# Kernel tuning notes

Hardware: AMD Instinct MI355X
Metric: run time of the kernel (lower is better)

The kernel has to match this reference:

```python
import jax, jax.numpy as jnp
import numpy as np

EPS = 1e-6  # flax LayerNorm default

def _layernorm(x, scale, bias):
    mu = jnp.mean(x, axis=-1, keepdims=True)
    var = jnp.mean(jnp.square(x - mu), axis=-1, keepdims=True)
    return (x - mu) * jax.lax.rsqrt(var + EPS) * scale + bias

def _rel_pos_index(ws):
    coords = np.stack(np.meshgrid(np.arange(ws), np.arange(ws), indexing='ij'))  # [2,ws,ws]
    cf = coords.reshape(2, -1)
    rel = (cf[:, :, None] - cf[:, None, :]).transpose(1, 2, 0)  # [N,N,2]
    rel[..., 0] += ws - 1
    rel[..., 1] += ws - 1
    rel[..., 0] *= 2 * ws - 1
    return rel.sum(-1)  # [N,N] in [0,(2ws-1)^2)

def setup_inputs() -> dict:
    key = jax.random.key(0)
    ks = jax.random.split(key, 8)
    B, H, W, C = 16, 56, 56, 384
    L, heads, ws = 2, 12, 7
    s = 0.02
    return {
        'x': jax.random.normal(ks[0], (B, H, W, C), jnp.float32),
        'ln1_s': jnp.ones((L, C), jnp.float32),
        'ln1_b': jnp.zeros((L, C), jnp.float32),
        'qkv_w': jax.random.normal(ks[1], (L, C, 3 * C), jnp.float32) * s,
        'rpb': jax.random.normal(ks[2], (L, (2 * ws - 1) ** 2, heads), jnp.float32) * s,
        'proj_w': jax.random.normal(ks[3], (L, C, C), jnp.float32) * s,
        'ln2_s': jnp.ones((L, C), jnp.float32),
        'ln2_b': jnp.zeros((L, C), jnp.float32),
        'mlp_w1': jax.random.normal(ks[4], (L, C, 4 * C), jnp.float32) * s,
        'mlp_b1': jnp.zeros((L, 4 * C), jnp.float32),
        'mlp_w2': jax.random.normal(ks[5], (L, 4 * C, C), jnp.float32) * s,
        'mlp_b2': jnp.zeros((L, C), jnp.float32),
        'window_size': 7,
    }

def reference(x, ln1_s, ln1_b, qkv_w, rpb, proj_w, ln2_s, ln2_b, mlp_w1, mlp_b1, mlp_w2, mlp_b2, window_size):
    B, H, W, C = x.shape
    ws = int(window_size)
    L = qkv_w.shape[0]
    heads = rpb.shape[-1]
    hd = C // heads
    N = ws * ws
    idx = jnp.asarray(_rel_pos_index(ws))  # [N,N] static

    # --- split to windows: [B,H,W,C] -> [B*nWh*nWw, N, C]
    xw = x.reshape(B, H // ws, ws, W // ws, ws, C)
    xw = xw.transpose(0, 1, 3, 2, 4, 5).reshape(-1, N, C)

    for l in range(L):
        # --- windowed MHSA with relative position bias
        h = _layernorm(xw, ln1_s[l], ln1_b[l])
        qkv = (h @ qkv_w[l]).reshape(-1, N, 3, heads, hd)
        q, k, v = qkv[:, :, 0], qkv[:, :, 1], qkv[:, :, 2]  # [nW,N,heads,hd]
        attn = jnp.einsum('wqhd,wkhd->whqk', q, k) * (hd ** -0.5)
        bias = rpb[l][idx].transpose(2, 0, 1)  # [heads,N,N]
        attn = jax.nn.softmax(attn + bias[None], axis=-1)
        o = jnp.einsum('whqk,wkhd->wqhd', attn, v).reshape(-1, N, C)
        xw = xw + o @ proj_w[l]
        # --- MLP block
        h = _layernorm(xw, ln2_s[l], ln2_b[l])
        h = jax.nn.gelu(h @ mlp_w1[l] + mlp_b1[l])
        xw = xw + (h @ mlp_w2[l] + mlp_b2[l])

    # --- merge windows back to [B,H,W,C]
    out = xw.reshape(B, H // ws, W // ws, ws, ws, C)
    out = out.transpose(0, 1, 3, 2, 4, 5).reshape(B, H, W, C)
    return out
```

## Files before the change

### kernel.cpp

```cpp
#include <hip/hip_runtime.h>
#include <hip/hip_bf16.h>

typedef __bf16 bf16;
typedef __attribute__((ext_vector_type(4))) __bf16 bf16x4;
typedef __attribute__((ext_vector_type(8))) __bf16 bf16x8;
typedef __attribute__((ext_vector_type(4))) float f32x4;

__device__ __forceinline__ void async_ld16(const void* g, void* l) {
    __builtin_amdgcn_global_load_lds(
        (const __attribute__((address_space(1))) unsigned int*)g,
        (__attribute__((address_space(3))) unsigned int*)l, 16, 0, 0);
}

__global__ __launch_bounds__(256) void k_f2bt(const float* __restrict__ in,
                                              bf16* __restrict__ out, int Kd, int Nd) {
    int id = blockIdx.x * 256 + threadIdx.x;
    if (id >= Kd * Nd) return;
    int k = id / Nd, n = id - k * Nd;
    out[(size_t)n * Kd + k] = (bf16)in[id];
}

__global__ __launch_bounds__(256) void k_reorder_in(const float4* __restrict__ x,
                                                    float4* __restrict__ xres) {
    int id = blockIdx.x * 256 + threadIdx.x;
    int c4 = id % 96;
    int t = id / 96;
    int b = t / 3136;
    int rem = t - b * 3136;
    int y = rem / 56;
    int xc = rem - y * 56;
    int w = b * 64 + (y / 7) * 8 + (xc / 7);
    int n = (y % 7) * 7 + (xc % 7);
    xres[(size_t)(w * 49 + n) * 96 + c4] = x[id];
}

__global__ __launch_bounds__(256) void k_reorder_out(const float4* __restrict__ xres,
                                                     float4* __restrict__ out) {
    int id = blockIdx.x * 256 + threadIdx.x;
    int c4 = id % 96;
    int t = id / 96;
    int b = t / 3136;
    int rem = t - b * 3136;
    int y = rem / 56;
    int xc = rem - y * 56;
    int w = b * 64 + (y / 7) * 8 + (xc / 7);
    int n = (y % 7) * 7 + (xc % 7);
    out[id] = xres[(size_t)(w * 49 + n) * 96 + c4];
}

__global__ __launch_bounds__(256) void k_ln(const float* __restrict__ xres,
                                            const float* __restrict__ s,
                                            const float* __restrict__ b,
                                            bf16* __restrict__ h) {
    int t = blockIdx.x * 4 + (threadIdx.x >> 6);
    int lane = threadIdx.x & 63;
    const float4* row = (const float4*)(xres + (size_t)t * 384);
    float4 v0 = row[lane];
    float4 v1 = make_float4(0.f, 0.f, 0.f, 0.f);
    if (lane < 32) v1 = row[64 + lane];
    float sum = v0.x + v0.y + v0.z + v0.w + v1.x + v1.y + v1.z + v1.w;
#pragma unroll
    for (int m = 1; m < 64; m <<= 1) sum += __shfl_xor(sum, m);
    float mu = sum * (1.f / 384.f);
    float sq = (v0.x - mu) * (v0.x - mu) + (v0.y - mu) * (v0.y - mu) +
               (v0.z - mu) * (v0.z - mu) + (v0.w - mu) * (v0.w - mu);
    if (lane < 32)
        sq += (v1.x - mu) * (v1.x - mu) + (v1.y - mu) * (v1.y - mu) +
              (v1.z - mu) * (v1.z - mu) + (v1.w - mu) * (v1.w - mu);
#pragma unroll
    for (int m = 1; m < 64; m <<= 1) sq += __shfl_xor(sq, m);
    float r = rsqrtf(sq * (1.f / 384.f) + 1e-6f);
    const float4* s4 = (const float4*)s;
    const float4* b4 = (const float4*)b;
    bf16* ho = h + (size_t)t * 384;
    {
        float4 sv = s4[lane], bv = b4[lane];
        bf16x4 ov;
        ov[0] = (bf16)((v0.x - mu) * r * sv.x + bv.x);
        ov[1] = (bf16)((v0.y - mu) * r * sv.y + bv.y);
        ov[2] = (bf16)((v0.z - mu) * r * sv.z + bv.z);
        ov[3] = (bf16)((v0.w - mu) * r * sv.w + bv.w);
        *(bf16x4*)&ho[lane * 4] = ov;
    }
    if (lane < 32) {
        float4 sv = s4[64 + lane], bv = b4[64 + lane];
        bf16x4 ov;
        ov[0] = (bf16)((v1.x - mu) * r * sv.x + bv.x);
        ov[1] = (bf16)((v1.y - mu) * r * sv.y + bv.y);
        ov[2] = (bf16)((v1.z - mu) * r * sv.z + bv.z);
        ov[3] = (bf16)((v1.w - mu) * r * sv.w + bv.w);
        *(bf16x4*)&ho[256 + lane * 4] = ov;
    }
}

__device__ inline float gelu_f(float x) {
    float u = 0.7978845608028654f * (x + 0.044715f * x * x * x);
    float t = 1.f - 2.f / (__expf(2.f * u) + 1.f);
    return 0.5f * x * (1.f + t);
}

template <int EPI>
__global__ __launch_bounds__(256) void k_gemm(const bf16* __restrict__ A,
                                              const bf16* __restrict__ Bt,
                                              const float* __restrict__ bias,
                                              float* __restrict__ resid,
                                              bf16* __restrict__ Cout,
                                              int N, int K) {
    __shared__ __align__(16) char lds[17408];
    bf16* As = (bf16*)lds;
    bf16* Bs = (bf16*)(lds + 8192);
    int tid = threadIdx.x;
    int n0 = blockIdx.x * 128;
    int m0 = blockIdx.y * 128;
    int wave = tid >> 6, lane = tid & 63;
    int wm = (wave >> 1) * 64, wn = (wave & 1) * 64;
    int col = lane & 15, quad = lane >> 4;

    f32x4 acc[4][4] = {};

    int r0 = 2 * wave * 16 + (lane >> 2);
    int ksl = (lane & 3) ^ ((r0 >> 1) & 3);
    const bf16* ga0 = A + (size_t)(m0 + r0) * K + ksl * 8;
    const bf16* gb0 = Bt + (size_t)(n0 + r0) * K + ksl * 8;
    size_t rowK16 = (size_t)16 * K;
    bf16* la0 = &As[2 * wave * 512];
    bf16* la1 = &As[(2 * wave + 1) * 512];
    bf16* lb0 = &Bs[2 * wave * 512];
    bf16* lb1 = &Bs[(2 * wave + 1) * 512];

    for (int kb = 0; kb < K; kb += 32) {
        __syncthreads();
        async_ld16(ga0 + kb, la0);
        async_ld16(ga0 + rowK16 + kb, la1);
        async_ld16(gb0 + kb, lb0);
        async_ld16(gb0 + rowK16 + kb, lb1);
        __syncthreads();

        bf16x8 af[4], bfv[4];
#pragma unroll
        for (int i = 0; i < 4; i++) {
            int ra = wm + i * 16 + col;
            af[i] = *(const bf16x8*)&As[ra * 32 + ((quad ^ ((ra >> 1) & 3)) << 3)];
            int rb = wn + i * 16 + col;
            bfv[i] = *(const bf16x8*)&Bs[rb * 32 + ((quad ^ ((rb >> 1) & 3)) << 3)];
        }
#pragma unroll
        for (int mi = 0; mi < 4; mi++)
#pragma unroll
            for (int ni = 0; ni < 4; ni++)
                acc[mi][ni] = __builtin_amdgcn_mfma_f32_16x16x32_bf16(
                    af[mi], bfv[ni], acc[mi][ni], 0, 0, 0);
    }

    __syncthreads();
    float* scrw = (float*)lds + wave * (16 * 68);

    int prow = lane >> 3;
    int pc0 = (lane & 7) * 8;
#pragma unroll
    for (int mi = 0; mi < 4; mi++) {
#pragma unroll
        for (int ni = 0; ni < 4; ni++)
#pragma unroll
            for (int r = 0; r < 4; r++)
                scrw[(quad * 4 + r) * 68 + ni * 16 + col] = acc[mi][ni][r];
#pragma unroll
        for (int h = 0; h < 2; h++) {
            int lr = h * 8 + prow;
            const float* sp = scrw + lr * 68 + pc0;
            float4 u0 = *(const float4*)sp;
            float4 u1 = *(const float4*)(sp + 4);
            int gm = m0 + wm + mi * 16 + lr;
            int gn = n0 + wn + pc0;
            size_t off = (size_t)gm * N + gn;
            if (EPI == 0) {
                bf16x8 ov;
                ov[0] = (bf16)u0.x; ov[1] = (bf16)u0.y; ov[2] = (bf16)u0.z; ov[3] = (bf16)u0.w;
                ov[4] = (bf16)u1.x; ov[5] = (bf16)u1.y; ov[6] = (bf16)u1.z; ov[7] = (bf16)u1.w;
                *(bf16x8*)&Cout[off] = ov;
            } else if (EPI == 1) {
                float4 b0 = *(const float4*)&bias[gn];
                float4 b1 = *(const float4*)&bias[gn + 4];
                bf16x8 ov;
                ov[0] = (bf16)gelu_f(u0.x + b0.x); ov[1] = (bf16)gelu_f(u0.y + b0.y);
                ov[2] = (bf16)gelu_f(u0.z + b0.z); ov[3] = (bf16)gelu_f(u0.w + b0.w);
                ov[4] = (bf16)gelu_f(u1.x + b1.x); ov[5] = (bf16)gelu_f(u1.y + b1.y);
                ov[6] = (bf16)gelu_f(u1.z + b1.z); ov[7] = (bf16)gelu_f(u1.w + b1.w);
                *(bf16x8*)&Cout[off] = ov;
            } else if (EPI == 2) {
                float4 r0v = *(const float4*)&resid[off];
                float4 r1v = *(const float4*)&resid[off + 4];
                r0v.x += u0.x; r0v.y += u0.y; r0v.z += u0.z; r0v.w += u0.w;
                r1v.x += u1.x; r1v.y += u1.y; r1v.z += u1.z; r1v.w += u1.w;
                *(float4*)&resid[off] = r0v;
                *(float4*)&resid[off + 4] = r1v;
            } else {
                float4 b0 = *(const float4*)&bias[gn];
                float4 b1 = *(const float4*)&bias[gn + 4];
                float4 r0v = *(const float4*)&resid[off];
                float4 r1v = *(const float4*)&resid[off + 4];
                r0v.x += u0.x + b0.x; r0v.y += u0.y + b0.y;
                r0v.z += u0.z + b0.z; r0v.w += u0.w + b0.w;
                r1v.x += u1.x + b1.x; r1v.y += u1.y + b1.y;
                r1v.z += u1.z + b1.z; r1v.w += u1.w + b1.w;
                *(float4*)&resid[off] = r0v;
                *(float4*)&resid[off + 4] = r1v;
            }
        }
    }
}

__global__ __launch_bounds__(256) void k_attn(const bf16* __restrict__ qkv,
                                              const float* __restrict__ rpb,
                                              bf16* __restrict__ o) {
    __shared__ unsigned short relIdx[2401];
    __shared__ float rpbs[4][169];
    __shared__ __align__(16) bf16 Vs[4][32 * 72];
    __shared__ __align__(16) bf16 Ps[4][64 * 72];

    int tid = threadIdx.x;
    int wave = tid >> 6, lane = tid & 63;
    int col = lane & 15, quad = lane >> 4;
    int w = blockIdx.x;
    int head = blockIdx.y * 4 + wave;
    const float scale = 0.17677669529663687f;

    for (int e = tid; e < 2401; e += 256) {
        int i = e / 49, j = e - i * 49;
        int yi = i / 7, xi = i - yi * 7, yj = j / 7, xj = j - yj * 7;
        relIdx[e] = (unsigned short)((yi - yj + 6) * 13 + (xi - xj + 6));
    }
    for (int e = lane; e < 169; e += 64) rpbs[wave][e] = rpb[e * 12 + head];

    const bf16* base = qkv + (size_t)w * 49 * 1152 + head * 32;
    bf16* vsw = Vs[wave];
    bf16* psw = Ps[wave];

    bf16x4 z4 = {(bf16)0.f, (bf16)0.f, (bf16)0.f, (bf16)0.f};
    for (int e = lane; e < 576; e += 64) *(bf16x4*)&vsw[e * 4] = z4;
    for (int e = lane; e < 392; e += 64) {
        int j = e >> 3, d4 = (e & 7) * 4;
        bf16x4 vv = *(const bf16x4*)&base[768 + (size_t)j * 1152 + d4];
        vsw[(d4 + 0) * 72 + j] = vv[0];
        vsw[(d4 + 1) * 72 + j] = vv[1];
        vsw[(d4 + 2) * 72 + j] = vv[2];
        vsw[(d4 + 3) * 72 + j] = vv[3];
    }

    __syncthreads();

    bf16x8 qf[4], kf[4];
#pragma unroll
    for (int mi = 0; mi < 4; mi++) {
        size_t row = (size_t)(mi * 16 + col) * 1152 + quad * 8;
        qf[mi] = *(const bf16x8*)&base[row];
        kf[mi] = *(const bf16x8*)&base[384 + row];
    }

    f32x4 S[4][4] = {};
#pragma unroll
    for (int mi = 0; mi < 4; mi++)
#pragma unroll
        for (int nj = 0; nj < 4; nj++)
            S[mi][nj] = __builtin_amdgcn_mfma_f32_16x16x32_bf16(qf[mi], kf[nj], S[mi][nj], 0, 0, 0);

    float* rp = rpbs[wave];
#pragma unroll
    for (int mi = 0; mi < 4; mi++) {
#pragma unroll
        for (int r = 0; r < 4; r++) {
            int ii = mi * 16 + quad * 4 + r;
            int ir = (ii < 49 ? ii : 0) * 49;
            float sv[4];
            float mx = -1e30f;
#pragma unroll
            for (int nj = 0; nj < 4; nj++) {
                int j = nj * 16 + col;
                float v;
                if (j < 49) v = S[mi][nj][r] * scale + rp[relIdx[ir + j]];
                else v = -1e30f;
                sv[nj] = v;
                mx = fmaxf(mx, v);
            }
#pragma unroll
            for (int m = 1; m < 16; m <<= 1) mx = fmaxf(mx, __shfl_xor(mx, m));
            float sum = 0.f;
#pragma unroll
            for (int nj = 0; nj < 4; nj++) {
                float p = __expf(sv[nj] - mx);
                sv[nj] = p;
                sum += p;
            }
#pragma unroll
            for (int m = 1; m < 16; m <<= 1) sum += __shfl_xor(sum, m);
            float is = 1.f / sum;
#pragma unroll
            for (int nj = 0; nj < 4; nj++)
                psw[ii * 72 + nj * 16 + col] = (bf16)(sv[nj] * is);
        }
    }

    __syncthreads();

    f32x4 O[4][2] = {};
#pragma unroll
    for (int kt = 0; kt < 2; kt++) {
        bf16x8 vb[2];
#pragma unroll
        for (int nt = 0; nt < 2; nt++)
            vb[nt] = *(const bf16x8*)&vsw[(nt * 16 + col) * 72 + kt * 32 + quad * 8];
#pragma unroll
        for (int mi = 0; mi < 4; mi++) {
            bf16x8 pa = *(const bf16x8*)&psw[(mi * 16 + col) * 72 + kt * 32 + quad * 8];
#pragma unroll
            for (int nt = 0; nt < 2; nt++)
                O[mi][nt] = __builtin_amdgcn_mfma_f32_16x16x32_bf16(pa, vb[nt], O[mi][nt], 0, 0, 0);
        }
    }

    bf16* ob = o + (size_t)w * 49 * 384 + head * 32;
#pragma unroll
    for (int mi = 0; mi < 4; mi++) {
#pragma unroll
        for (int r = 0; r < 4; r++) {
            int i = mi * 16 + quad * 4 + r;
            if (i < 49) {
#pragma unroll
                for (int nt = 0; nt < 2; nt++)
                    ob[(size_t)i * 384 + nt * 16 + col] = (bf16)O[mi][nt][r];
            }
        }
    }
}

extern "C" void kernel_launch(void* const* d_in, const int* in_sizes, int n_in,
                              void* d_out, int out_size, void* d_ws, size_t ws_size,
                              hipStream_t stream) {
    const float* x      = (const float*)d_in[0];
    const float* ln1_s  = (const float*)d_in[1];
    const float* ln1_b  = (const float*)d_in[2];
    const float* qkv_w  = (const float*)d_in[3];
    const float* rpb    = (const float*)d_in[4];
    const float* proj_w = (const float*)d_in[5];
    const float* ln2_s  = (const float*)d_in[6];
    const float* ln2_b  = (const float*)d_in[7];
    const float* mlp_w1 = (const float*)d_in[8];
    const float* mlp_b1 = (const float*)d_in[9];
    const float* mlp_w2 = (const float*)d_in[10];
    const float* mlp_b2 = (const float*)d_in[11];
    float* out = (float*)d_out;

    char* ws = (char*)d_ws;
    float* xres  = (float*)ws;
    bf16* qkvbuf = (bf16*)(ws + 77070336);
    bf16* obuf   = (bf16*)(ws + 192675840);
    bf16* wbuf   = (bf16*)(ws + 231211008);
    bf16* hidden = qkvbuf;
    bf16* hbuf   = (bf16*)d_out;

    bf16* qkvw_b  = wbuf;
    bf16* projw_b = wbuf + 884736;
    bf16* mlp1_b  = wbuf + 1179648;
    bf16* mlp2_b  = wbuf + 2359296;

    for (int l = 0; l < 2; l++) {
        k_f2bt<<<1728, 256, 0, stream>>>(qkv_w + (size_t)l * 442368,
                                         qkvw_b + (size_t)l * 442368, 384, 1152);
        k_f2bt<<<576, 256, 0, stream>>>(proj_w + (size_t)l * 147456,
                                        projw_b + (size_t)l * 147456, 384, 384);
        k_f2bt<<<2304, 256, 0, stream>>>(mlp_w1 + (size_t)l * 589824,
                                         mlp1_b + (size_t)l * 589824, 384, 1536);
        k_f2bt<<<2304, 256, 0, stream>>>(mlp_w2 + (size_t)l * 589824,
                                         mlp2_b + (size_t)l * 589824, 1536, 384);
    }

    k_reorder_in<<<18816, 256, 0, stream>>>((const float4*)x, (float4*)xres);

    for (int l = 0; l < 2; l++) {
        k_ln<<<12544, 256, 0, stream>>>(xres, ln1_s + l * 384, ln1_b + l * 384, hbuf);
        k_gemm<0><<<dim3(9, 392), 256, 0, stream>>>(
            hbuf, qkvw_b + (size_t)l * 442368, nullptr, nullptr, qkvbuf, 1152, 384);
        k_attn<<<dim3(1024, 3), 256, 0, stream>>>(qkvbuf, rpb + l * 169 * 12, obuf);
        k_gemm<2><<<dim3(3, 392), 256, 0, stream>>>(
            obuf, projw_b + (size_t)l * 147456, nullptr, xres, nullptr, 384, 384);
        k_ln<<<12544, 256, 0, stream>>>(xres, ln2_s + l * 384, ln2_b + l * 384, hbuf);
        k_gemm<1><<<dim3(12, 392), 256, 0, stream>>>(
            hbuf, mlp1_b + (size_t)l * 589824, mlp_b1 + l * 1536, nullptr, hidden, 1536, 384);
        k_gemm<3><<<dim3(3, 392), 256, 0, stream>>>(
            hidden, mlp2_b + (size_t)l * 589824, mlp_b2 + l * 384, xres, nullptr, 384, 1536);
    }

    k_reorder_out<<<18816, 256, 0, stream>>>((const float4*)xres, (float4*)out);
}
```

Baseline: 1.248 ms.

## Fuse LayerNorm and window reorder into residual GEMM epilogues

Adds a full-row GEMM kernel (64 rows by all 384 output columns per block) that applies the residual add and then computes the next LayerNorm from the fresh outputs, writing both the fp32 residual and the bf16 normalized activations. The first LayerNorm is fused with the window-partition reorder, and the last MLP2 GEMM scatters straight into the un-windowed output layout. This removes the standalone LN and reorder kernels and their extra passes over the fp32 activations. In exchange the fused GEMM has only 784 blocks, a larger LDS footprint and single-buffered loads, uses one-pass variance, and does scalar uncoalesced residual and output accesses.

```diff
diff --git a/kernel.cpp b/kernel.cpp
--- a/kernel.cpp
+++ b/kernel.cpp
@@ -20,41 +20,21 @@
     out[(size_t)n * Kd + k] = (bf16)in[id];
 }
 
-__global__ __launch_bounds__(256) void k_reorder_in(const float4* __restrict__ x,
-                                                    float4* __restrict__ xres) {
-    int id = blockIdx.x * 256 + threadIdx.x;
-    int c4 = id % 96;
-    int t = id / 96;
-    int b = t / 3136;
-    int rem = t - b * 3136;
-    int y = rem / 56;
-    int xc = rem - y * 56;
-    int w = b * 64 + (y / 7) * 8 + (xc / 7);
+__global__ __launch_bounds__(256) void k_lnr(const float* __restrict__ x,
+                                             const float* __restrict__ s,
+                                             const float* __restrict__ b,
+                                             float* __restrict__ xres,
+                                             bf16* __restrict__ h) {
+    int traw = blockIdx.x * 4 + (threadIdx.x >> 6);
+    int lane = threadIdx.x & 63;
+    int bb = traw / 3136;
+    int rem = traw - bb * 3136;
+    int y = rem / 56, xc = rem - y * 56;
+    int w = bb * 64 + (y / 7) * 8 + (xc / 7);
     int n = (y % 7) * 7 + (xc % 7);
-    xres[(size_t)(w * 49 + n) * 96 + c4] = x[id];
-}
-
-__global__ __launch_bounds__(256) void k_reorder_out(const float4* __restrict__ xres,
-                                                     float4* __restrict__ out) {
-    int id = blockIdx.x * 256 + threadIdx.x;
-    int c4 = id % 96;
-    int t = id / 96;
-    int b = t / 3136;
-    int rem = t - b * 3136;
-    int y = rem / 56;
-    int xc = rem - y * 56;
-    int w = b * 64 + (y / 7) * 8 + (xc / 7);
-    int n = (y % 7) * 7 + (xc % 7);
-    out[id] = xres[(size_t)(w * 49 + n) * 96 + c4];
-}
-
-__global__ __launch_bounds__(256) void k_ln(const float* __restrict__ xres,
-                                            const float* __restrict__ s,
-                                            const float* __restrict__ b,
-                                            bf16* __restrict__ h) {
-    int t = blockIdx.x * 4 + (threadIdx.x >> 6);
-    int lane = threadIdx.x & 63;
-    const float4* row = (const float4*)(xres + (size_t)t * 384);
+    int twin = w * 49 + n;
+
+    const float4* row = (const float4*)(x + (size_t)traw * 384);
     float4 v0 = row[lane];
     float4 v1 = make_float4(0.f, 0.f, 0.f, 0.f);
     if (lane < 32) v1 = row[64 + lane];
@@ -70,10 +50,13 @@
 #pragma unroll
     for (int m = 1; m < 64; m <<= 1) sq += __shfl_xor(sq, m);
     float r = rsqrtf(sq * (1.f / 384.f) + 1e-6f);
+
+    float4* xr = (float4*)(xres + (size_t)twin * 384);
     const float4* s4 = (const float4*)s;
     const float4* b4 = (const float4*)b;
-    bf16* ho = h + (size_t)t * 384;
+    bf16* ho = h + (size_t)twin * 384;
     {
+        xr[lane] = v0;
         float4 sv = s4[lane], bv = b4[lane];
         bf16x4 ov;
         ov[0] = (bf16)((v0.x - mu) * r * sv.x + bv.x);
@@ -83,6 +66,7 @@
         *(bf16x4*)&ho[lane * 4] = ov;
     }
     if (lane < 32) {
+        xr[64 + lane] = v1;
         float4 sv = s4[64 + lane], bv = b4[64 + lane];
         bf16x4 ov;
         ov[0] = (bf16)((v1.x - mu) * r * sv.x + bv.x);
@@ -103,7 +87,6 @@
 __global__ __launch_bounds__(256) void k_gemm(const bf16* __restrict__ A,
                                               const bf16* __restrict__ Bt,
                                               const float* __restrict__ bias,
-                                              float* __restrict__ resid,
                                               bf16* __restrict__ Cout,
                                               int N, int K) {
     __shared__ __align__(16) char lds[17408];
@@ -178,7 +161,7 @@
                 ov[0] = (bf16)u0.x; ov[1] = (bf16)u0.y; ov[2] = (bf16)u0.z; ov[3] = (bf16)u0.w;
                 ov[4] = (bf16)u1.x; ov[5] = (bf16)u1.y; ov[6] = (bf16)u1.z; ov[7] = (bf16)u1.w;
                 *(bf16x8*)&Cout[off] = ov;
-            } else if (EPI == 1) {
+            } else {
                 float4 b0 = *(const float4*)&bias[gn];
                 float4 b1 = *(const float4*)&bias[gn + 4];
                 bf16x8 ov;
@@ -187,24 +170,146 @@
                 ov[4] = (bf16)gelu_f(u1.x + b1.x); ov[5] = (bf16)gelu_f(u1.y + b1.y);
                 ov[6] = (bf16)gelu_f(u1.z + b1.z); ov[7] = (bf16)gelu_f(u1.w + b1.w);
                 *(bf16x8*)&Cout[off] = ov;
-            } else if (EPI == 2) {
-                float4 r0v = *(const float4*)&resid[off];
-                float4 r1v = *(const float4*)&resid[off + 4];
-                r0v.x += u0.x; r0v.y += u0.y; r0v.z += u0.z; r0v.w += u0.w;
-                r1v.x += u1.x; r1v.y += u1.y; r1v.z += u1.z; r1v.w += u1.w;
-                *(float4*)&resid[off] = r0v;
-                *(float4*)&resid[off + 4] = r1v;
-            } else {
-                float4 b0 = *(const float4*)&bias[gn];
-                float4 b1 = *(const float4*)&bias[gn + 4];
-                float4 r0v = *(const float4*)&resid[off];
-                float4 r1v = *(const float4*)&resid[off + 4];
-                r0v.x += u0.x + b0.x; r0v.y += u0.y + b0.y;
-                r0v.z += u0.z + b0.z; r0v.w += u0.w + b0.w;
-                r1v.x += u1.x + b1.x; r1v.y += u1.y + b1.y;
-                r1v.z += u1.z + b1.z; r1v.w += u1.w + b1.w;
-                *(float4*)&resid[off] = r0v;
-                *(float4*)&resid[off + 4] = r1v;
+            }
+        }
+    }
+}
+
+template <int MODE>
+__global__ __launch_bounds__(256) void k_gemm_ln(const bf16* __restrict__ A,
+                                                 const bf16* __restrict__ Bt,
+                                                 const float* __restrict__ bias,
+                                                 float* __restrict__ resid,
+                                                 const float* __restrict__ lns,
+                                                 const float* __restrict__ lnb,
+                                                 bf16* __restrict__ hout,
+                                                 float* __restrict__ outp,
+                                                 int K) {
+    __shared__ __align__(16) bf16 As[64 * 32];
+    __shared__ __align__(16) bf16 Bs[384 * 32];
+    __shared__ float pstat[64][4][2];
+    __shared__ float sS[384], bS[384], biasS[384];
+    int tid = threadIdx.x;
+    int wave = tid >> 6, lane = tid & 63;
+    int col = lane & 15, quad = lane >> 4;
+    int m0 = blockIdx.x * 64;
+    int j0 = wave * 96;
+
+    for (int t = tid; t < 384; t += 256) {
+        if (MODE != 2) { sS[t] = lns[t]; bS[t] = lnb[t]; }
+        if (MODE != 0) biasS[t] = bias[t];
+    }
+
+    f32x4 acc[4][6] = {};
+
+    int arow = 16 * wave + (lane >> 2);
+    int aks = ((lane & 3) ^ ((arow >> 1) & 3)) << 3;
+    const bf16* ga = A + (size_t)(m0 + arow) * K + aks;
+    bf16* la = &As[wave * 512];
+    const bf16* gb[6];
+    bf16* lb[6];
+#pragma unroll
+    for (int c = 0; c < 6; c++) {
+        int brow = 16 * (wave + 4 * c) + (lane >> 2);
+        int bks = ((lane & 3) ^ ((brow >> 1) & 3)) << 3;
+        gb[c] = Bt + (size_t)brow * K + bks;
+        lb[c] = &Bs[(wave + 4 * c) * 512];
+    }
+
+    for (int kb = 0; kb < K; kb += 32) {
+        __syncthreads();
+        async_ld16(ga + kb, la);
+#pragma unroll
+        for (int c = 0; c < 6; c++) async_ld16(gb[c] + kb, lb[c]);
+        __syncthreads();
+
+        bf16x8 af[4], bfv[6];
+#pragma unroll
+        for (int i = 0; i < 4; i++) {
+            int ra = i * 16 + col;
+            af[i] = *(const bf16x8*)&As[ra * 32 + ((quad ^ ((ra >> 1) & 3)) << 3)];
+        }
+#pragma unroll
+        for (int i = 0; i < 6; i++) {
+            int rb = j0 + i * 16 + col;
+            bfv[i] = *(const bf16x8*)&Bs[rb * 32 + ((quad ^ ((rb >> 1) & 3)) << 3)];
+        }
+#pragma unroll
+        for (int mi = 0; mi < 4; mi++)
+#pragma unroll
+            for (int ni = 0; ni < 6; ni++)
+                acc[mi][ni] = __builtin_amdgcn_mfma_f32_16x16x32_bf16(
+                    af[mi], bfv[ni], acc[mi][ni], 0, 0, 0);
+    }
+
+#pragma unroll
+    for (int mi = 0; mi < 4; mi++) {
+        float psum[4] = {0.f, 0.f, 0.f, 0.f};
+        float psq[4] = {0.f, 0.f, 0.f, 0.f};
+#pragma unroll
+        for (int ni = 0; ni < 6; ni++) {
+            int j = j0 + ni * 16 + col;
+            float bv = (MODE == 0) ? 0.f : biasS[j];
+            size_t off = (size_t)(m0 + mi * 16 + quad * 4) * 384 + j;
+#pragma unroll
+            for (int r = 0; r < 4; r++) {
+                float v = acc[mi][ni][r] + bv + resid[off + (size_t)r * 384];
+                acc[mi][ni][r] = v;
+                if (MODE != 2) {
+                    resid[off + (size_t)r * 384] = v;
+                    psum[r] += v;
+                    psq[r] += v * v;
+                }
+            }
+        }
+        if (MODE != 2) {
+#pragma unroll
+            for (int r = 0; r < 4; r++) {
+#pragma unroll
+                for (int m = 1; m < 16; m <<= 1) {
+                    psum[r] += __shfl_xor(psum[r], m);
+                    psq[r] += __shfl_xor(psq[r], m);
+                }
+                if (col == 0) {
+                    int il = mi * 16 + quad * 4 + r;
+                    pstat[il][wave][0] = psum[r];
+                    pstat[il][wave][1] = psq[r];
+                }
+            }
+        } else {
+#pragma unroll
+            for (int r = 0; r < 4; r++) {
+                int gm = m0 + mi * 16 + quad * 4 + r;
+                int w = gm / 49, n = gm - w * 49;
+                int bb = w >> 6, r64 = w & 63;
+                int yy = (r64 >> 3) * 7 + n / 7;
+                int xx = (r64 & 7) * 7 + n % 7;
+                size_t traw = ((size_t)((bb * 56 + yy) * 56 + xx)) * 384;
+#pragma unroll
+                for (int ni = 0; ni < 6; ni++)
+                    outp[traw + j0 + ni * 16 + col] = acc[mi][ni][r];
+            }
+        }
+    }
+
+    if (MODE != 2) {
+        __syncthreads();
+#pragma unroll
+        for (int mi = 0; mi < 4; mi++) {
+#pragma unroll
+            for (int r = 0; r < 4; r++) {
+                int il = mi * 16 + quad * 4 + r;
+                float s = pstat[il][0][0] + pstat[il][1][0] + pstat[il][2][0] + pstat[il][3][0];
+                float sq = pstat[il][0][1] + pstat[il][1][1] + pstat[il][2][1] + pstat[il][3][1];
+                float mu = s * (1.f / 384.f);
+                float var = fmaxf(sq * (1.f / 384.f) - mu * mu, 0.f);
+                float rstd = rsqrtf(var + 1e-6f);
+                size_t ho = (size_t)(m0 + il) * 384;
+#pragma unroll
+                for (int ni = 0; ni < 6; ni++) {
+                    int j = j0 + ni * 16 + col;
+                    hout[ho + j] = (bf16)((acc[mi][ni][r] - mu) * rstd * sS[j] + bS[j]);
+                }
             }
         }
     }
@@ -374,21 +479,25 @@
                                          mlp2_b + (size_t)l * 589824, 1536, 384);
     }
 
-    k_reorder_in<<<18816, 256, 0, stream>>>((const float4*)x, (float4*)xres);
+    k_lnr<<<12544, 256, 0, stream>>>(x, ln1_s, ln1_b, xres, hbuf);
 
     for (int l = 0; l < 2; l++) {
-        k_ln<<<12544, 256, 0, stream>>>(xres, ln1_s + l * 384, ln1_b + l * 384, hbuf);
         k_gemm<0><<<dim3(9, 392), 256, 0, stream>>>(
-            hbuf, qkvw_b + (size_t)l * 442368, nullptr, nullptr, qkvbuf, 1152, 384);
-        k_attn<<<dim3(1024, 3), 256, 0, stream>>>(qkvbuf, rpb + l * 169 * 12, obuf);
-        k_gemm<2><<<dim3(3, 392), 256, 0, stream>>>(
-            obuf, projw_b + (size_t)l * 147456, nullptr, xres, nullptr, 384, 384);
-        k_ln<<<12544, 256, 0, stream>>>(xres, ln2_s + l * 384, ln2_b + l * 384, hbuf);
+            hbuf, qkvw_b + (size_t)l * 442368, nullptr, qkvbuf, 1152, 384);
+        k_attn<<<dim3(1024, 3), 256, 0, stream>>>(qkvbuf, rpb + l * 2028, obuf);
+        k_gemm_ln<0><<<784, 256, 0, stream>>>(
+            obuf, projw_b + (size_t)l * 147456, nullptr, xres,
+            ln2_s + l * 384, ln2_b + l * 384, hbuf, nullptr, 384);
         k_gemm<1><<<dim3(12, 392), 256, 0, stream>>>(
-            hbuf, mlp1_b + (size_t)l * 589824, mlp_b1 + l * 1536, nullptr, hidden, 1536, 384);
-        k_gemm<3><<<dim3(3, 392), 256, 0, stream>>>(
-            hidden, mlp2_b + (size_t)l * 589824, mlp_b2 + l * 384, xres, nullptr, 384, 1536);
-    }
-
-    k_reorder_out<<<18816, 256, 0, stream>>>((const float4*)xres, (float4*)out);
-}
+            hbuf, mlp1_b + (size_t)l * 589824, mlp_b1 + l * 1536, hidden, 1536, 384);
+        if (l == 0) {
+            k_gemm_ln<1><<<784, 256, 0, stream>>>(
+                hidden, mlp2_b, mlp_b2, xres,
+                ln1_s + 384, ln1_b + 384, hbuf, nullptr, 1536);
+        } else {
+            k_gemm_ln<2><<<784, 256, 0, stream>>>(
+                hidden, mlp2_b + 589824, mlp_b2 + 384, xres,
+                nullptr, nullptr, nullptr, out, 1536);
+        }
+    }
+}
```

After: 1.384 ms. +10.9%, slower.
